# Performance work log

Measured on AMD Instinct MI355X. Metric: run time of the kernel, lower is better.

Reference implementation:

```python
import jax, jax.numpy as jnp
import numpy as np

N_NODES = 10000
N_EDGES = 80000
OBS_DIMS = 128
HIDDEN = 1024
ACT_DIMS = 8
N_GRAPHS = 64


def setup_inputs() -> dict:
    key = jax.random.key(0)
    ks = jax.random.split(key, 8)
    x = jax.random.normal(ks[0], (N_NODES, OBS_DIMS), dtype=jnp.float32)
    edge_index = jax.random.randint(ks[1], (2, N_EDGES), 0, N_NODES, dtype=jnp.int64)
    batch = jnp.sort(jax.random.randint(ks[2], (N_NODES,), 0, N_GRAPHS, dtype=jnp.int64))
    # Glorot-style init for weights, zero bias (as in PyG GCNConv / Linear defaults)
    W1 = jax.random.normal(ks[3], (OBS_DIMS, HIDDEN), dtype=jnp.float32) * (1.0 / np.sqrt(OBS_DIMS))
    b1 = jnp.zeros((HIDDEN,), dtype=jnp.float32)
    W2 = jax.random.normal(ks[4], (HIDDEN, HIDDEN), dtype=jnp.float32) * (1.0 / np.sqrt(HIDDEN))
    b2 = jnp.zeros((HIDDEN,), dtype=jnp.float32)
    Wl = jax.random.normal(ks[5], (HIDDEN, ACT_DIMS), dtype=jnp.float32) * (1.0 / np.sqrt(HIDDEN))
    bl = jnp.zeros((ACT_DIMS,), dtype=jnp.float32)
    return {"x": x, "edge_index": edge_index, "batch": batch,
            "W1": W1, "b1": b1, "W2": W2, "b2": b2, "Wl": Wl, "bl": bl}


def _gcn_conv(x, src, dst, dinv, W, b, n):
    """PyG GCNConv: D^-1/2 (A+I) D^-1/2 X W + b (self-loops already in src/dst)."""
    h = x @ W                                   # [N, out]
    norm = (dinv[src] * dinv[dst])[:, None]      # [E+N, 1]
    msg = h[src] * norm                          # gather + scale
    out = jax.ops.segment_sum(msg, dst, num_segments=n)
    return out + b


def reference(x, edge_index, batch, W1, b1, W2, b2, Wl, bl):
    n = x.shape[0]
    loops = jnp.arange(n, dtype=edge_index.dtype)
    src = jnp.concatenate([edge_index[0], loops])  # add self-loops
    dst = jnp.concatenate([edge_index[1], loops])
    # degree (with self-loops) from destination column, as PyG does
    deg = jax.ops.segment_sum(jnp.ones_like(dst, dtype=x.dtype), dst, num_segments=n)
    dinv = jax.lax.rsqrt(jnp.maximum(deg, 1.0))

    h = jax.nn.relu(_gcn_conv(x, src, dst, dinv, W1, b1, n))
    h = _gcn_conv(h, src, dst, dinv, W2, b2, n)
    h = jnp.tanh(h @ Wl + bl)                    # [N, act_dims]

    # global_mean_pool over batch segment ids
    sums = jax.ops.segment_sum(h, batch, num_segments=N_GRAPHS)
    counts = jax.ops.segment_sum(jnp.ones((n, 1), h.dtype), batch, num_segments=N_GRAPHS)
    return sums / jnp.maximum(counts, 1.0)       # [N_GRAPHS, act_dims]
```

## Files before the change

kernel.cpp:

```cpp
#include <hip/hip_runtime.h>
#include <hip/hip_bf16.h>

#define NNODES 10000
#define NEDGES 80000
#define OBS    128
#define HID    1024
#define ACTD   8
#define NGR    64

typedef __bf16 bf16x8 __attribute__((ext_vector_type(8)));
typedef float  f32x4  __attribute__((ext_vector_type(4)));
typedef const __attribute__((address_space(1))) unsigned int gl_u32;
typedef __attribute__((address_space(3))) unsigned int lds_u32;

__device__ __forceinline__ ushort f2b(float f) {
    union { float f; unsigned int i; } v; v.f = f;
    unsigned int lsb = (v.i >> 16) & 1u;
    unsigned int r = v.i + 0x7fffu + lsb;
    return (ushort)(r >> 16);
}
__device__ __forceinline__ int cix(int v, int hi) {
    return v < 0 ? 0 : (v >= hi ? hi - 1 : v);
}

__global__ __launch_bounds__(256) void k_prep(const float* __restrict__ W1,
                                              const float* __restrict__ W2,
                                              const float* __restrict__ Wl,
                                              const float* __restrict__ b2,
                                              const float* __restrict__ bl,
                                              ushort* __restrict__ Wt1,
                                              ushort* __restrict__ M2bf,
                                              float* __restrict__ b2l,
                                              float* __restrict__ zacc,
                                              float* __restrict__ pool,
                                              float* __restrict__ cnt,
                                              int* __restrict__ degi) {
    int blk = blockIdx.x;
    if (blk >= 385) {
        int idx = (blk - 385) * 256 + threadIdx.x;
        if (idx < NNODES * ACTD) zacc[idx] = 0.0f;
        if (idx < NGR * ACTD) pool[idx] = 0.0f;
        if (idx < NGR) cnt[idx] = 0.0f;
        if (idx < NNODES) degi[idx] = 0;
        return;
    }
    if (blk < 128) {
        __shared__ float tile[32][33];
        int bx = (blk & 31) * 32, by = (blk >> 5) * 32;
        int tx = threadIdx.x & 31, ty = threadIdx.x >> 5;
        #pragma unroll
        for (int i = 0; i < 32; i += 8)
            tile[ty + i][tx] = W1[(size_t)(by + ty + i) * HID + bx + tx];
        __syncthreads();
        #pragma unroll
        for (int i = 0; i < 32; i += 8)
            Wt1[(size_t)(bx + ty + i) * OBS + by + tx] = f2b(tile[tx][ty + i]);
        return;
    }
    int wvid = ((blk - 128) * 256 + (int)threadIdx.x) >> 6;
    int lane = threadIdx.x & 63;
    if (wvid > HID) return;
    const float* row = (wvid == HID) ? b2 : (W2 + (size_t)wvid * HID);
    float acc[ACTD];
    #pragma unroll
    for (int j = 0; j < ACTD; ++j) acc[j] = 0.0f;
    for (int it = 0; it < HID / 64; ++it) {
        int k = it * 64 + lane;
        float w2v = row[k];
        float4 a = *(const float4*)(Wl + (size_t)k * ACTD);
        float4 b = *(const float4*)(Wl + (size_t)k * ACTD + 4);
        acc[0] += w2v * a.x; acc[1] += w2v * a.y; acc[2] += w2v * a.z; acc[3] += w2v * a.w;
        acc[4] += w2v * b.x; acc[5] += w2v * b.y; acc[6] += w2v * b.z; acc[7] += w2v * b.w;
    }
    #pragma unroll
    for (int off = 32; off > 0; off >>= 1)
        #pragma unroll
        for (int j = 0; j < ACTD; ++j)
            acc[j] += __shfl_down(acc[j], off);
    if (lane == 0) {
        if (wvid == HID) {
            #pragma unroll
            for (int j = 0; j < ACTD; ++j) b2l[j] = acc[j] + bl[j];
        } else {
            #pragma unroll
            for (int j = 0; j < ACTD; ++j) M2bf[wvid * ACTD + j] = f2b(acc[j]);
        }
    }
}

__global__ void k_count(const int* __restrict__ dst, int* degi, int e) {
    int i = blockIdx.x * 256 + threadIdx.x;
    if (i < e) atomicAdd(&degi[cix(dst[i], NNODES)], 1);
}

__global__ __launch_bounds__(1024) void k_scan(const int* __restrict__ degi,
                                               int* rowptr, int* cursor, float* dinv) {
    __shared__ int wsum[16];
    int t = threadIdx.x, lane = t & 63, w = t >> 6;
    int base = t * 10;
    int local[10];
    int s = 0;
    #pragma unroll
    for (int k = 0; k < 10; ++k) {
        int i = base + k;
        int v = 0;
        if (i < NNODES) {
            v = degi[i];
            dinv[i] = rsqrtf((float)(v + 1));
        }
        local[k] = s; s += v;
    }
    int sc = s;
    #pragma unroll
    for (int off = 1; off < 64; off <<= 1) {
        int u = __shfl_up(sc, off);
        if (lane >= off) sc += u;
    }
    if (lane == 63) wsum[w] = sc;
    __syncthreads();
    if (w == 0 && lane < 16) {
        int v = wsum[lane];
        #pragma unroll
        for (int off = 1; off < 16; off <<= 1) {
            int u = __shfl_up(v, off);
            if (lane >= off) v += u;
        }
        wsum[lane] = v;
    }
    __syncthreads();
    int excl = ((w == 0) ? 0 : wsum[w - 1]) + (sc - s);
    #pragma unroll
    for (int k = 0; k < 10; ++k) {
        int i = base + k;
        if (i < NNODES) { rowptr[i] = excl + local[k]; cursor[i] = excl + local[k]; }
    }
    if (t == 0) rowptr[NNODES] = wsum[15];
}

__global__ void k_fill(const int* __restrict__ src, const int* __restrict__ dst,
                       const float* __restrict__ dinv, int* cursor,
                       int* __restrict__ esrc, float* __restrict__ coefs, int e) {
    int i = blockIdx.x * 256 + threadIdx.x;
    if (i >= e) return;
    int s = cix(src[i], NNODES), d = cix(dst[i], NNODES);
    int pos = atomicAdd(&cursor[d], 1);
    esrc[pos] = s;
    coefs[pos] = dinv[s] * dinv[d];
}

__global__ void k_aggx(const float* __restrict__ x, const float* __restrict__ dinv,
                       const int* __restrict__ rowptr, const int* __restrict__ esrc,
                       const float* __restrict__ coefs, ushort* __restrict__ aggbf, int n) {
    int wv = (blockIdx.x * 256 + threadIdx.x) >> 6;
    int lane = threadIdx.x & 63;
    if (wv >= n) return;
    float d = dinv[wv], d2 = d * d;
    float2 xv = *(const float2*)(x + (size_t)wv * OBS + lane * 2);
    float v0 = xv.x * d2, v1 = xv.y * d2;
    int e = rowptr[wv], e1 = rowptr[wv + 1];
    for (; e + 2 <= e1; e += 2) {
        int s0 = esrc[e], s1 = esrc[e + 1];
        float c0 = coefs[e], c1 = coefs[e + 1];
        float2 a = *(const float2*)(x + (size_t)s0 * OBS + lane * 2);
        float2 b = *(const float2*)(x + (size_t)s1 * OBS + lane * 2);
        v0 += a.x * c0 + b.x * c1;
        v1 += a.y * c0 + b.y * c1;
    }
    if (e < e1) {
        int s0 = esrc[e];
        float c0 = coefs[e];
        float2 a = *(const float2*)(x + (size_t)s0 * OBS + lane * 2);
        v0 += a.x * c0; v1 += a.y * c0;
    }
    ushort2 o; o.x = f2b(v0); o.y = f2b(v1);
    *(ushort2*)(aggbf + (size_t)wv * OBS + lane * 2) = o;
}

__global__ __launch_bounds__(256) void k_gemm1_fused(const ushort* __restrict__ A,
                                                     const ushort* __restrict__ Bt,
                                                     const float* __restrict__ bias,
                                                     const ushort* __restrict__ M2bf,
                                                     float* __restrict__ zacc,
                                                     int M) {
    __shared__ ushort buf[128 * 136 + 16 * 128];
    ushort* As    = buf;
    ushort* Bs    = buf + 8192;
    ushort* stage = buf;
    ushort* M2t   = buf + 128 * 136;

    const int t = threadIdx.x;
    const int bm = blockIdx.x, bn = blockIdx.y;
    const int lane = t & 63, wv = t >> 6;
    const int wm = (wv & 1) * 64, wn = (wv >> 1) * 64;
    const int l16 = lane & 15, kg = (lane >> 4) * 8;

    if (t < 128) {
        ushort4 a = *(const ushort4*)(M2bf + (size_t)(bn * 128 + t) * ACTD);
        ushort4 b = *(const ushort4*)(M2bf + (size_t)(bn * 128 + t) * ACTD + 4);
        M2t[0 * 128 + t] = a.x; M2t[1 * 128 + t] = a.y;
        M2t[2 * 128 + t] = a.z; M2t[3 * 128 + t] = a.w;
        M2t[4 * 128 + t] = b.x; M2t[5 * 128 + t] = b.y;
        M2t[6 * 128 + t] = b.z; M2t[7 * 128 + t] = b.w;
        #pragma unroll
        for (int j = 8; j < 16; ++j) M2t[j * 128 + t] = 0;
    }

    f32x4 acc[4][4];
    #pragma unroll
    for (int i = 0; i < 4; ++i)
        #pragma unroll
        for (int j = 0; j < 4; ++j)
            acc[i][j] = (f32x4){0.f, 0.f, 0.f, 0.f};

    const int rs = t >> 3;
    const int cs = (t & 7) * 8;
    #pragma unroll
    for (int kt = 0; kt < OBS; kt += 64) {
        #pragma unroll
        for (int p = 0; p < 4; ++p) {
            int r = rs + p * 32;
            int gr = bm * 128 + r; if (gr >= M) gr = M - 1;
            __builtin_amdgcn_global_load_lds(
                (gl_u32*)(A + (size_t)gr * OBS + kt + cs),
                (lds_u32*)(As + r * 64 + cs), 16, 0, 0);
            int gn = bn * 128 + r;
            __builtin_amdgcn_global_load_lds(
                (gl_u32*)(Bt + (size_t)gn * OBS + kt + cs),
                (lds_u32*)(Bs + r * 64 + cs), 16, 0, 0);
        }
        __syncthreads();
        #pragma unroll
        for (int k2 = 0; k2 < 64; k2 += 32) {
            bf16x8 af[4], bfr[4];
            #pragma unroll
            for (int i = 0; i < 4; ++i)
                af[i] = *(const bf16x8*)(As + (wm + i * 16 + l16) * 64 + k2 + kg);
            #pragma unroll
            for (int j = 0; j < 4; ++j)
                bfr[j] = *(const bf16x8*)(Bs + (wn + j * 16 + l16) * 64 + k2 + kg);
            #pragma unroll
            for (int i = 0; i < 4; ++i)
                #pragma unroll
                for (int j = 0; j < 4; ++j)
                    acc[i][j] = __builtin_amdgcn_mfma_f32_16x16x32_bf16(af[i], bfr[j], acc[i][j], 0, 0, 0);
        }
        __syncthreads();
    }

    #pragma unroll
    for (int i = 0; i < 4; ++i) {
        int rowb = wm + i * 16 + (lane >> 4) * 4;
        #pragma unroll
        for (int j = 0; j < 4; ++j) {
            int col = wn + j * 16 + l16;
            float bj = bias[bn * 128 + col];
            #pragma unroll
            for (int r = 0; r < 4; ++r)
                stage[(rowb + r) * 136 + col] = f2b(fmaxf(acc[i][j][r] + bj, 0.0f));
        }
    }
    __syncthreads();

    #pragma unroll
    for (int st = 0; st < 2; ++st) {
        int row0 = wv * 32 + st * 16;
        f32x4 z = (f32x4){0.f, 0.f, 0.f, 0.f};
        #pragma unroll
        for (int kt = 0; kt < 128; kt += 32) {
            bf16x8 a = *(const bf16x8*)(stage + (row0 + l16) * 136 + kt + kg);
            bf16x8 b = *(const bf16x8*)(M2t + l16 * 128 + kt + kg);
            z = __builtin_amdgcn_mfma_f32_16x16x32_bf16(a, b, z, 0, 0, 0);
        }
        if (l16 < ACTD) {
            int rowb = bm * 128 + row0 + (lane >> 4) * 4;
            #pragma unroll
            for (int r = 0; r < 4; ++r)
                if (rowb + r < M)
                    atomicAdd(&zacc[(size_t)(rowb + r) * ACTD + l16], z[r]);
        }
    }
}

__global__ __launch_bounds__(1024) void k_zfinal(const float* __restrict__ zacc,
                                                 const float* __restrict__ dinv,
                                                 const int* __restrict__ rowptr,
                                                 const int* __restrict__ esrc,
                                                 const float* __restrict__ coefs,
                                                 const float* __restrict__ b2l,
                                                 const int* __restrict__ batch,
                                                 float* __restrict__ pool,
                                                 float* __restrict__ cnt, int n) {
    __shared__ float part[NGR * ACTD];
    __shared__ int   partc[NGR];
    int t = threadIdx.x;
    if (t < NGR * ACTD) part[t] = 0.0f;
    if (t < NGR) partc[t] = 0;
    __syncthreads();

    int idx = blockIdx.x * 1024 + t;
    int i = idx >> 3, j = idx & 7;
    if (i < n) {
        float d = dinv[i];
        float v = zacc[idx] * d * d;
        int e0 = rowptr[i], e1 = rowptr[i + 1];
        for (int e = e0; e < e1; ++e)
            v += coefs[e] * zacc[(size_t)esrc[e] * ACTD + j];
        float tz = tanhf(v + b2l[j]);
        int g = cix(batch[i], NGR);
        atomicAdd(&part[g * ACTD + j], tz);
        if (j == 0) atomicAdd(&partc[g], 1);
    }
    __syncthreads();

    int i0 = (blockIdx.x * 1024) >> 3;
    int i1 = (blockIdx.x * 1024 + 1023) >> 3;
    if (i0 >= n) return;
    if (i1 >= n) i1 = n - 1;
    int g0 = cix(batch[i0], NGR), g1 = cix(batch[i1], NGR);
    int ng = g1 - g0 + 1;
    if (t < ng * ACTD)
        atomicAdd(&pool[g0 * ACTD + t], part[g0 * ACTD + t]);
    if (t < ng) {
        int c = partc[g0 + t];
        if (c) atomicAdd(&cnt[g0 + t], (float)c);
    }
}

__global__ void k_final(const float* __restrict__ pool, const float* __restrict__ cnt,
                        float* __restrict__ out, int total) {
    int i = blockIdx.x * 256 + threadIdx.x;
    if (i < total) out[i] = pool[i] / fmaxf(cnt[i >> 3], 1.0f);
}

extern "C" void kernel_launch(void* const* d_in, const int* in_sizes, int n_in,
                              void* d_out, int out_size, void* d_ws, size_t ws_size,
                              hipStream_t stream) {
    const float* x   = (const float*)d_in[0];
    const int*   ei  = (const int*)d_in[1];
    const int*   bat = (const int*)d_in[2];
    const float* W1  = (const float*)d_in[3];
    const float* b1  = (const float*)d_in[4];
    const float* W2  = (const float*)d_in[5];
    const float* b2v = (const float*)d_in[6];
    const float* Wl  = (const float*)d_in[7];
    const float* bl  = (const float*)d_in[8];
    float* out = (float*)d_out;

    const int N = NNODES, E = NEDGES;
    const int* src = ei;
    const int* dst = ei + E;

    char* ws = (char*)d_ws;
    size_t off = 0;
    float*  pool   = (float*)(ws + off); off += 2048;
    float*  cnt    = (float*)(ws + off); off += 256;
    float*  dinv   = (float*)(ws + off); off += 40192;
    int*    degi   = (int*)(ws + off);   off += 40192;
    int*    rowptr = (int*)(ws + off);   off += 40448;
    int*    cursor = (int*)(ws + off);   off += 40192;
    int*    esrc   = (int*)(ws + off);   off += (size_t)E * 4;
    float*  coefs  = (float*)(ws + off); off += (size_t)E * 4;
    float*  b2l    = (float*)(ws + off); off += 256;
    ushort* M2bf   = (ushort*)(ws + off); off += (size_t)HID * ACTD * 2;
    ushort* Wt1    = (ushort*)(ws + off); off += (size_t)HID * OBS * 2;
    float*  zacc   = (float*)(ws + off); off += (size_t)N * ACTD * 4;
    ushort* aggbf  = (ushort*)(ws + off); off += (size_t)N * OBS * 2;

    k_prep<<<698, 256, 0, stream>>>(W1, W2, Wl, b2v, bl, Wt1, M2bf, b2l,
                                    zacc, pool, cnt, degi);
    k_count<<<(E + 255) / 256, 256, 0, stream>>>(dst, degi, E);
    k_scan<<<1, 1024, 0, stream>>>(degi, rowptr, cursor, dinv);
    k_fill<<<(E + 255) / 256, 256, 0, stream>>>(src, dst, dinv, cursor, esrc, coefs, E);

    k_aggx<<<(N * 64 + 255) / 256, 256, 0, stream>>>(x, dinv, rowptr, esrc, coefs, aggbf, N);

    k_gemm1_fused<<<dim3((N + 127) / 128, HID / 128), 256, 0, stream>>>(
        aggbf, Wt1, b1, M2bf, zacc, N);

    k_zfinal<<<(N * ACTD + 1023) / 1024, 1024, 0, stream>>>(
        zacc, dinv, rowptr, esrc, coefs, b2l, bat, pool, cnt, N);
    k_final<<<2, 256, 0, stream>>>(pool, cnt, out, NGR * ACTD);
}
```

Before: 134.3 us.

## Fuse graph build into cooperative kernel, merge final divide, widen aggregation loads

Replaces the separate count, scan and fill kernels with one cooperative kernel that uses grid-wide syncs and a two-level parallel scan. This removes launch gaps and the single-block serial scan. The final mean-divide kernel is folded into k_zfinal through a last-block-done counter, and k_zfinal moves to 256-thread blocks. k_aggx now splits each node's edges across two half-waves using float4 loads and combines them with a shuffle. The trade-off is cooperative-launch and grid-sync overhead, plus more atomics on pool from the larger number of blocks.

```diff
diff --git a/kernel.cpp b/kernel.cpp
--- a/kernel.cpp
+++ b/kernel.cpp
@@ -1,5 +1,8 @@
 #include <hip/hip_runtime.h>
 #include <hip/hip_bf16.h>
+#include <hip/hip_cooperative_groups.h>
+
+namespace cg = cooperative_groups;
 
 #define NNODES 10000
 #define NEDGES 80000
@@ -34,7 +37,8 @@
                                               float* __restrict__ zacc,
                                               float* __restrict__ pool,
                                               float* __restrict__ cnt,
-                                              int* __restrict__ degi) {
+                                              int* __restrict__ degi,
+                                              int* __restrict__ done) {
     int blk = blockIdx.x;
     if (blk >= 385) {
         int idx = (blk - 385) * 256 + threadIdx.x;
@@ -42,6 +46,7 @@
         if (idx < NGR * ACTD) pool[idx] = 0.0f;
         if (idx < NGR) cnt[idx] = 0.0f;
         if (idx < NNODES) degi[idx] = 0;
+        if (idx == 0) *done = 0;
         return;
     }
     if (blk < 128) {
@@ -88,64 +93,73 @@
     }
 }
 
-__global__ void k_count(const int* __restrict__ dst, int* degi, int e) {
-    int i = blockIdx.x * 256 + threadIdx.x;
-    if (i < e) atomicAdd(&degi[cix(dst[i], NNODES)], 1);
-}
-
-__global__ __launch_bounds__(1024) void k_scan(const int* __restrict__ degi,
-                                               int* rowptr, int* cursor, float* dinv) {
-    __shared__ int wsum[16];
-    int t = threadIdx.x, lane = t & 63, w = t >> 6;
-    int base = t * 10;
-    int local[10];
-    int s = 0;
-    #pragma unroll
-    for (int k = 0; k < 10; ++k) {
-        int i = base + k;
+__global__ __launch_bounds__(256) void k_graph(const int* __restrict__ src,
+                                               const int* __restrict__ dst,
+                                               int* __restrict__ degi,
+                                               float* __restrict__ dinv,
+                                               int* __restrict__ rowptr,
+                                               int* __restrict__ cursor,
+                                               int* __restrict__ chunksum,
+                                               int* __restrict__ esrc,
+                                               float* __restrict__ coefs,
+                                               int e) {
+    cg::grid_group grid = cg::this_grid();
+    const int t = threadIdx.x, b = blockIdx.x;
+    const int gid = b * 256 + t;
+
+    if (gid < e) atomicAdd(&degi[cix(dst[gid], NNODES)], 1);
+    grid.sync();
+
+    __shared__ int wsum[4];
+    if (b < 40) {
+        int i = b * 256 + t;
         int v = 0;
+        if (i < NNODES) { v = degi[i]; dinv[i] = rsqrtf((float)(v + 1)); }
+        int lane = t & 63, w = t >> 6;
+        int sc = v;
+        #pragma unroll
+        for (int off = 1; off < 64; off <<= 1) {
+            int u = __shfl_up(sc, off);
+            if (lane >= off) sc += u;
+        }
+        if (lane == 63) wsum[w] = sc;
+        __syncthreads();
+        int wo = 0;
+        #pragma unroll
+        for (int k = 0; k < 4; ++k) if (k < w) wo += wsum[k];
+        if (i < NNODES) rowptr[i] = wo + sc - v;
+        if (t == 255) chunksum[b] = wo + sc;
+    }
+    grid.sync();
+
+    if (b == 0 && t < 64) {
+        int v = (t < 40) ? chunksum[t] : 0;
+        int sc = v;
+        #pragma unroll
+        for (int off = 1; off < 64; off <<= 1) {
+            int u = __shfl_up(sc, off);
+            if (t >= off) sc += u;
+        }
+        if (t < 40) chunksum[t] = sc - v;
+        if (t == 39) rowptr[NNODES] = sc;
+    }
+    grid.sync();
+
+    if (b < 40) {
+        int i = b * 256 + t;
         if (i < NNODES) {
-            v = degi[i];
-            dinv[i] = rsqrtf((float)(v + 1));
-        }
-        local[k] = s; s += v;
-    }
-    int sc = s;
-    #pragma unroll
-    for (int off = 1; off < 64; off <<= 1) {
-        int u = __shfl_up(sc, off);
-        if (lane >= off) sc += u;
-    }
-    if (lane == 63) wsum[w] = sc;
-    __syncthreads();
-    if (w == 0 && lane < 16) {
-        int v = wsum[lane];
-        #pragma unroll
-        for (int off = 1; off < 16; off <<= 1) {
-            int u = __shfl_up(v, off);
-            if (lane >= off) v += u;
-        }
-        wsum[lane] = v;
-    }
-    __syncthreads();
-    int excl = ((w == 0) ? 0 : wsum[w - 1]) + (sc - s);
-    #pragma unroll
-    for (int k = 0; k < 10; ++k) {
-        int i = base + k;
-        if (i < NNODES) { rowptr[i] = excl + local[k]; cursor[i] = excl + local[k]; }
-    }
-    if (t == 0) rowptr[NNODES] = wsum[15];
-}
-
-__global__ void k_fill(const int* __restrict__ src, const int* __restrict__ dst,
-                       const float* __restrict__ dinv, int* cursor,
-                       int* __restrict__ esrc, float* __restrict__ coefs, int e) {
-    int i = blockIdx.x * 256 + threadIdx.x;
-    if (i >= e) return;
-    int s = cix(src[i], NNODES), d = cix(dst[i], NNODES);
-    int pos = atomicAdd(&cursor[d], 1);
-    esrc[pos] = s;
-    coefs[pos] = dinv[s] * dinv[d];
+            int r = rowptr[i] + chunksum[b];
+            rowptr[i] = r; cursor[i] = r;
+        }
+    }
+    grid.sync();
+
+    if (gid < e) {
+        int s = cix(src[gid], NNODES), d = cix(dst[gid], NNODES);
+        int pos = atomicAdd(&cursor[d], 1);
+        esrc[pos] = s;
+        coefs[pos] = dinv[s] * dinv[d];
+    }
 }
 
 __global__ void k_aggx(const float* __restrict__ x, const float* __restrict__ dinv,
@@ -154,26 +168,30 @@
     int wv = (blockIdx.x * 256 + threadIdx.x) >> 6;
     int lane = threadIdx.x & 63;
     if (wv >= n) return;
-    float d = dinv[wv], d2 = d * d;
-    float2 xv = *(const float2*)(x + (size_t)wv * OBS + lane * 2);
-    float v0 = xv.x * d2, v1 = xv.y * d2;
-    int e = rowptr[wv], e1 = rowptr[wv + 1];
-    for (; e + 2 <= e1; e += 2) {
-        int s0 = esrc[e], s1 = esrc[e + 1];
-        float c0 = coefs[e], c1 = coefs[e + 1];
-        float2 a = *(const float2*)(x + (size_t)s0 * OBS + lane * 2);
-        float2 b = *(const float2*)(x + (size_t)s1 * OBS + lane * 2);
-        v0 += a.x * c0 + b.x * c1;
-        v1 += a.y * c0 + b.y * c1;
-    }
-    if (e < e1) {
-        int s0 = esrc[e];
-        float c0 = coefs[e];
-        float2 a = *(const float2*)(x + (size_t)s0 * OBS + lane * 2);
-        v0 += a.x * c0; v1 += a.y * c0;
-    }
-    ushort2 o; o.x = f2b(v0); o.y = f2b(v1);
-    *(ushort2*)(aggbf + (size_t)wv * OBS + lane * 2) = o;
+    int half = lane >> 5, c = lane & 31;
+    float d = dinv[wv];
+    float4 v = make_float4(0.f, 0.f, 0.f, 0.f);
+    if (half == 0) {
+        float d2 = d * d;
+        float4 xs = *(const float4*)(x + (size_t)wv * OBS + c * 4);
+        v.x = xs.x * d2; v.y = xs.y * d2; v.z = xs.z * d2; v.w = xs.w * d2;
+    }
+    int e1 = rowptr[wv + 1];
+    for (int e = rowptr[wv] + half; e < e1; e += 2) {
+        int s = esrc[e];
+        float cf = coefs[e];
+        float4 a = *(const float4*)(x + (size_t)s * OBS + c * 4);
+        v.x += a.x * cf; v.y += a.y * cf; v.z += a.z * cf; v.w += a.w * cf;
+    }
+    v.x += __shfl_down(v.x, 32);
+    v.y += __shfl_down(v.y, 32);
+    v.z += __shfl_down(v.z, 32);
+    v.w += __shfl_down(v.w, 32);
+    if (half == 0) {
+        ushort4 o;
+        o.x = f2b(v.x); o.y = f2b(v.y); o.z = f2b(v.z); o.w = f2b(v.w);
+        *(ushort4*)(aggbf + (size_t)wv * OBS + c * 4) = o;
+    }
 }
 
 __global__ __launch_bounds__(256) void k_gemm1_fused(const ushort* __restrict__ A,
@@ -281,23 +299,26 @@
     }
 }
 
-__global__ __launch_bounds__(1024) void k_zfinal(const float* __restrict__ zacc,
-                                                 const float* __restrict__ dinv,
-                                                 const int* __restrict__ rowptr,
-                                                 const int* __restrict__ esrc,
-                                                 const float* __restrict__ coefs,
-                                                 const float* __restrict__ b2l,
-                                                 const int* __restrict__ batch,
-                                                 float* __restrict__ pool,
-                                                 float* __restrict__ cnt, int n) {
+__global__ __launch_bounds__(256) void k_zfinal(const float* __restrict__ zacc,
+                                                const float* __restrict__ dinv,
+                                                const int* __restrict__ rowptr,
+                                                const int* __restrict__ esrc,
+                                                const float* __restrict__ coefs,
+                                                const float* __restrict__ b2l,
+                                                const int* __restrict__ batch,
+                                                float* __restrict__ pool,
+                                                float* __restrict__ cnt,
+                                                int* __restrict__ done,
+                                                float* __restrict__ out, int n) {
     __shared__ float part[NGR * ACTD];
     __shared__ int   partc[NGR];
+    __shared__ int   lastblk;
     int t = threadIdx.x;
-    if (t < NGR * ACTD) part[t] = 0.0f;
+    part[t] = 0.0f; part[t + 256] = 0.0f;
     if (t < NGR) partc[t] = 0;
     __syncthreads();
 
-    int idx = blockIdx.x * 1024 + t;
+    int idx = blockIdx.x * 256 + t;
     int i = idx >> 3, j = idx & 7;
     if (i < n) {
         float d = dinv[i];
@@ -312,24 +333,33 @@
     }
     __syncthreads();
 
-    int i0 = (blockIdx.x * 1024) >> 3;
-    int i1 = (blockIdx.x * 1024 + 1023) >> 3;
-    if (i0 >= n) return;
+    int i0 = (blockIdx.x * 256) >> 3;
+    int i1 = (blockIdx.x * 256 + 255) >> 3;
     if (i1 >= n) i1 = n - 1;
     int g0 = cix(batch[i0], NGR), g1 = cix(batch[i1], NGR);
     int ng = g1 - g0 + 1;
-    if (t < ng * ACTD)
-        atomicAdd(&pool[g0 * ACTD + t], part[g0 * ACTD + t]);
-    if (t < ng) {
-        int c = partc[g0 + t];
-        if (c) atomicAdd(&cnt[g0 + t], (float)c);
-    }
-}
-
-__global__ void k_final(const float* __restrict__ pool, const float* __restrict__ cnt,
-                        float* __restrict__ out, int total) {
-    int i = blockIdx.x * 256 + threadIdx.x;
-    if (i < total) out[i] = pool[i] / fmaxf(cnt[i >> 3], 1.0f);
+    for (int u = t; u < ng * ACTD; u += 256)
+        atomicAdd(&pool[g0 * ACTD + u], part[g0 * ACTD + u]);
+    for (int u = t; u < ng; u += 256) {
+        int c = partc[g0 + u];
+        if (c) atomicAdd(&cnt[g0 + u], (float)c);
+    }
+
+    __threadfence();
+    __syncthreads();
+    if (t == 0) {
+        unsigned old = __hip_atomic_fetch_add((unsigned int*)done, 1u,
+                                              __ATOMIC_ACQ_REL, __HIP_MEMORY_SCOPE_AGENT);
+        lastblk = (old == (unsigned)(gridDim.x - 1));
+    }
+    __syncthreads();
+    if (lastblk) {
+        for (int u = t; u < NGR * ACTD; u += 256) {
+            float p = __hip_atomic_load(&pool[u], __ATOMIC_RELAXED, __HIP_MEMORY_SCOPE_AGENT);
+            float c = __hip_atomic_load(&cnt[u >> 3], __ATOMIC_RELAXED, __HIP_MEMORY_SCOPE_AGENT);
+            out[u] = p / fmaxf(c, 1.0f);
+        }
+    }
 }
 
 extern "C" void kernel_launch(void* const* d_in, const int* in_sizes, int n_in,
@@ -346,7 +376,7 @@
     const float* bl  = (const float*)d_in[8];
     float* out = (float*)d_out;
 
-    const int N = NNODES, E = NEDGES;
+    int N = NNODES, E = NEDGES;
     const int* src = ei;
     const int* dst = ei + E;
 
@@ -365,19 +395,25 @@
     ushort* Wt1    = (ushort*)(ws + off); off += (size_t)HID * OBS * 2;
     float*  zacc   = (float*)(ws + off); off += (size_t)N * ACTD * 4;
     ushort* aggbf  = (ushort*)(ws + off); off += (size_t)N * OBS * 2;
+    int*    chunks = (int*)(ws + off);   off += 256;
+    int*    done   = (int*)(ws + off);   off += 256;
 
     k_prep<<<698, 256, 0, stream>>>(W1, W2, Wl, b2v, bl, Wt1, M2bf, b2l,
-                                    zacc, pool, cnt, degi);
-    k_count<<<(E + 255) / 256, 256, 0, stream>>>(dst, degi, E);
-    k_scan<<<1, 1024, 0, stream>>>(degi, rowptr, cursor, dinv);
-    k_fill<<<(E + 255) / 256, 256, 0, stream>>>(src, dst, dinv, cursor, esrc, coefs, E);
+                                    zacc, pool, cnt, degi, done);
+
+    {
+        void* args[] = {(void*)&src, (void*)&dst, (void*)&degi, (void*)&dinv,
+                        (void*)&rowptr, (void*)&cursor, (void*)&chunks,
+                        (void*)&esrc, (void*)&coefs, (void*)&E};
+        hipLaunchCooperativeKernel((void*)k_graph, dim3(320), dim3(256),
+                                   args, 0, stream);
+    }
 
     k_aggx<<<(N * 64 + 255) / 256, 256, 0, stream>>>(x, dinv, rowptr, esrc, coefs, aggbf, N);
 
     k_gemm1_fused<<<dim3((N + 127) / 128, HID / 128), 256, 0, stream>>>(
         aggbf, Wt1, b1, M2bf, zacc, N);
 
-    k_zfinal<<<(N * ACTD + 1023) / 1024, 1024, 0, stream>>>(
-        zacc, dinv, rowptr, esrc, coefs, b2l, bat, pool, cnt, N);
-    k_final<<<2, 256, 0, stream>>>(pool, cnt, out, NGR * ACTD);
-}
+    k_zfinal<<<(N * ACTD + 255) / 256, 256, 0, stream>>>(
+        zacc, dinv, rowptr, esrc, coefs, b2l, bat, pool, cnt, done, out, N);
+}
```

Measured after the change: 304.2 us. 2.26x slower.
